# Performance work log

Hardware: AMD Instinct MI355X
Metric: run time of the kernel (lower is better)

Reference implementation:

```python
import jax, jax.numpy as jnp
import numpy as np

N = 100000
E = 3200000
G = 2000
EPS = 1e-5

def gcn_conv(x, W, b, src, dst):
    # PyG GCNConv: add self-loops, symmetric deg^-1/2 normalization,
    # out_i = sum_j norm_ij * (x_j @ W) + b
    loop = jnp.arange(N, dtype=src.dtype)
    s = jnp.concatenate([src, loop])
    d = jnp.concatenate([dst, loop])
    deg = jax.ops.segment_sum(jnp.ones_like(d, dtype=x.dtype), d, num_segments=N)
    dinv = jax.lax.rsqrt(jnp.maximum(deg, 1.0))
    norm = dinv[s] * dinv[d]                      # [E+N]
    h = x @ W                                     # [N, out]
    msg = h[s] * norm[:, None]                    # gather + scale
    return jax.ops.segment_sum(msg, d, num_segments=N) + b

def batchnorm(h, g, be):
    mu = jnp.mean(h, axis=0)
    var = jnp.mean((h - mu) ** 2, axis=0)
    return (h - mu) * jax.lax.rsqrt(var + EPS) * g + be

def setup_inputs() -> dict:
    key = jax.random.key(0)
    ks = jax.random.split(key, 16)
    inp = {
        "x": jax.random.normal(ks[0], (N, 10), dtype=jnp.float32),
        "src": jax.random.randint(ks[1], (E,), 0, N, dtype=jnp.int32),
        "dst": jax.random.randint(ks[2], (E,), 0, N, dtype=jnp.int32),
        "batch": jnp.sort(jax.random.randint(ks[3], (N,), 0, G, dtype=jnp.int32)),
        "W1": jax.random.normal(ks[4], (10, 64), dtype=jnp.float32) * 0.3,
        "b1": jnp.zeros((64,), jnp.float32),
        "g1": jnp.ones((64,), jnp.float32),
        "be1": jnp.zeros((64,), jnp.float32),
        "W2": jax.random.normal(ks[5], (64, 128), dtype=jnp.float32) * 0.12,
        "b2": jnp.zeros((128,), jnp.float32),
        "g2": jnp.ones((128,), jnp.float32),
        "be2": jnp.zeros((128,), jnp.float32),
        "fW1": jax.random.normal(ks[6], (128, 64), dtype=jnp.float32) * 0.09,
        "fb1": jnp.zeros((64,), jnp.float32),
        "fW2": jax.random.normal(ks[7], (64, 1), dtype=jnp.float32) * 0.12,
        "fb2": jnp.zeros((1,), jnp.float32),
    }
    return inp

def reference(x, src, dst, batch, W1, b1, g1, be1, W2, b2, g2, be2, fW1, fb1, fW2, fb2):
    h = jax.nn.relu(batchnorm(gcn_conv(x, W1, b1, src, dst), g1, be1))
    h = jax.nn.relu(batchnorm(gcn_conv(h, W2, b2, src, dst), g2, be2))
    # global_mean_pool over graphs
    s = jax.ops.segment_sum(h, batch, num_segments=G)
    cnt = jax.ops.segment_sum(jnp.ones((N,), h.dtype), batch, num_segments=G)
    pooled = s / jnp.maximum(cnt, 1.0)[:, None]   # [G, 128]
    # dropout is identity in eval mode
    h = jax.nn.relu(pooled @ fW1 + fb1)
    return h @ fW2 + fb2                          # [G, 1]
```

## Files before the change

kernel.cpp:

```cpp
#include <hip/hip_runtime.h>
#include <hip/hip_fp16.h>

#define NN 100000
#define NE 3200000
#define NG 2000
#define NB 391
#define BKT_SH 8
#define EPB 2048
#define EPT (EPB / 256)
#define PAD 16
#define CAP 10240
static constexpr float BN_EPS = 1e-5f;

typedef _Float16 f16x8 __attribute__((ext_vector_type(8)));
typedef float    f32x4 __attribute__((ext_vector_type(4)));

__global__ __launch_bounds__(1024) void k_init(int* bcur, float* s1, float* s2) {
    int t = threadIdx.x;
    if (t < NB) bcur[t * PAD] = t * CAP;
    if (t < 128) s1[t] = 0.f;
    if (t < 256) s2[t] = 0.f;
}

__global__ __launch_bounds__(256) void k_bucket(const int* __restrict__ src, const int* __restrict__ dst,
                                                int* __restrict__ bcur, int* __restrict__ stage) {
    __shared__ int cnt[NB];
    __shared__ int base[NB];
    int t = threadIdx.x;
    long long e0 = (long long)blockIdx.x * EPB;
    int ew[EPT], eb[EPT], lp[EPT];
#pragma unroll
    for (int i = 0; i < EPT; ++i) {
        long long e = e0 + t + i * 256;
        if (e < NE) {
            int d = dst[e];
            ew[i] = ((d & 255) << 17) | src[e];
            eb[i] = d >> BKT_SH;
        } else eb[i] = -1;
    }
    for (int i = t; i < NB; i += 256) cnt[i] = 0;
    __syncthreads();
#pragma unroll
    for (int i = 0; i < EPT; ++i)
        if (eb[i] >= 0) lp[i] = atomicAdd(&cnt[eb[i]], 1);
    __syncthreads();
    for (int i = t; i < NB; i += 256) {
        int c = cnt[i];
        base[i] = c ? atomicAdd(&bcur[i * PAD], c) : 0;
    }
    __syncthreads();
#pragma unroll
    for (int i = 0; i < EPT; ++i)
        if (eb[i] >= 0) stage[base[eb[i]] + lp[i]] = ew[i];
}

__global__ __launch_bounds__(256) void k_csr(const int* __restrict__ stage,
                                             const int* __restrict__ bcur, const float* __restrict__ x,
                                             int* __restrict__ deg_i, int* __restrict__ row_start,
                                             float* __restrict__ dinv, int* __restrict__ srcs,
                                             __half2* __restrict__ xh2) {
    __shared__ int ldeg[256];
    __shared__ int scn[256];
    __shared__ int lcur[256];
    int t = threadIdx.x;
    int b = blockIdx.x;
    int base = b * CAP;
    int end  = bcur[b * PAD];
    ldeg[t] = 0;
    __syncthreads();
    for (int e = base + t; e < end; e += 256)
        atomicAdd(&ldeg[(stage[e] >> 17) & 255], 1);
    __syncthreads();
    int v = ldeg[t];
    scn[t] = v;
    __syncthreads();
#pragma unroll
    for (int off = 1; off < 256; off <<= 1) {
        int a = (t >= off) ? scn[t - off] : 0;
        __syncthreads();
        scn[t] += a;
        __syncthreads();
    }
    int rs = base + scn[t] - v;
    lcur[t] = rs;
    int i = (b << BKT_SH) + t;
    if (i < NN) {
        deg_i[i] = v;
        row_start[i] = rs;
        float dv = rsqrtf((float)(v + 1));
        dinv[i] = dv;
        float xv[10];
#pragma unroll
        for (int k = 0; k < 10; ++k) xv[k] = x[i * 10 + k] * dv;
#pragma unroll
        for (int c = 0; c < 8; ++c) {
            float a = (2 * c < 10) ? xv[2 * c] : 0.f;
            float bb = (2 * c + 1 < 10) ? xv[2 * c + 1] : 0.f;
            xh2[i * 8 + c] = __floats2half2_rn(a, bb);
        }
    }
    __syncthreads();
    for (int e = base + t; e < end; e += 256) {
        int w = stage[e];
        int pos = atomicAdd(&lcur[(w >> 17) & 255], 1);
        srcs[pos] = w & 0x1FFFF;
    }
}

__global__ __launch_bounds__(256) void k_gather1(const __half2* __restrict__ xh2, const int* __restrict__ srcs,
                                                 const int* __restrict__ row_start, const int* __restrict__ deg,
                                                 const float* __restrict__ dinv, float2* __restrict__ aggx2) {
    int lane = threadIdx.x & 63;
    int wid  = threadIdx.x >> 6;
    int sub  = lane >> 3;
    int li   = lane & 7;
    int d = blockIdx.x * 32 + wid * 8 + sub;
    if (d >= NN) return;
    int start = row_start[d];
    int cnt   = deg[d];
    float ax = 0.f, ay = 0.f;
    int k = 0;
    for (; k + 4 <= cnt; k += 4) {
        int s0 = srcs[start + k];
        int s1 = srcs[start + k + 1];
        int s2 = srcs[start + k + 2];
        int s3 = srcs[start + k + 3];
        float2 u0 = __half22float2(xh2[s0 * 8 + li]);
        float2 u1 = __half22float2(xh2[s1 * 8 + li]);
        float2 u2 = __half22float2(xh2[s2 * 8 + li]);
        float2 u3 = __half22float2(xh2[s3 * 8 + li]);
        ax += (u0.x + u1.x) + (u2.x + u3.x);
        ay += (u0.y + u1.y) + (u2.y + u3.y);
    }
    for (; k < cnt; ++k) {
        int s = srcs[start + k];
        float2 u = __half22float2(xh2[s * 8 + li]);
        ax += u.x; ay += u.y;
    }
    {
        float2 u = __half22float2(xh2[d * 8 + li]);
        ax += u.x; ay += u.y;
    }
    float dd = dinv[d];
    aggx2[d * 8 + li] = make_float2(dd * ax, dd * ay);
}

__global__ __launch_bounds__(256) void k_mm1s(const float* __restrict__ aggx, const float* __restrict__ W,
                                              const float* __restrict__ b, __half* __restrict__ h1h,
                                              float* __restrict__ sums1) {
    __shared__ float ls[256];
    __shared__ float lq[256];
    int t = threadIdx.x;
    int rg = t >> 6;
    int f = t & 63;
    float w[10];
#pragma unroll
    for (int k = 0; k < 10; ++k) w[k] = W[k * 64 + f];
    float bf = b[f];
    float s = 0.f, q = 0.f;
    for (int row = blockIdx.x * 4 + rg; row < NN; row += 512 * 4) {
        float acc = bf;
#pragma unroll
        for (int k = 0; k < 10; ++k) acc += aggx[row * 16 + k] * w[k];
        s += acc; q += acc * acc;
        h1h[row * 64 + f] = __float2half(acc);
    }
    ls[t] = s; lq[t] = q;
    __syncthreads();
    if (t < 64) {
        float S = ls[t] + ls[t + 64] + ls[t + 128] + ls[t + 192];
        float Q = lq[t] + lq[t + 64] + lq[t + 128] + lq[t + 192];
        atomicAdd(&sums1[f], S);
        atomicAdd(&sums1[64 + f], Q);
    }
}

__global__ __launch_bounds__(256) void k_bn_apply1h(const float4* __restrict__ h1h4, const float* __restrict__ sums1,
                                                    const float* __restrict__ g, const float* __restrict__ be,
                                                    const float* __restrict__ dinv, int2* __restrict__ h1f8) {
    int idx = blockIdx.x * 256 + threadIdx.x;
    if (idx >= NN * 8) return;
    int i = idx >> 3;
    int c = idx & 7;
    const float invn = 1.0f / (float)NN;
    float dv = dinv[i];
    float4 r = h1h4[idx];
    const __half2* p = (const __half2*)&r;
    float rv[8];
#pragma unroll
    for (int j = 0; j < 4; ++j) {
        int f0 = 8 * c + 2 * j, f1 = f0 + 1;
        float mu0 = sums1[f0] * invn, mu1 = sums1[f1] * invn;
        float sc0 = g[f0] * rsqrtf(sums1[64 + f0] * invn - mu0 * mu0 + BN_EPS);
        float sc1 = g[f1] * rsqrtf(sums1[64 + f1] * invn - mu1 * mu1 + BN_EPS);
        float2 u = __half22float2(p[j]);
        rv[2 * j]     = fmaxf((u.x - mu0) * sc0 + be[f0], 0.f) * dv;
        rv[2 * j + 1] = fmaxf((u.y - mu1) * sc1 + be[f1], 0.f) * dv;
    }
    int lo = __builtin_amdgcn_cvt_pk_fp8_f32(rv[0], rv[1], 0, false);
    lo     = __builtin_amdgcn_cvt_pk_fp8_f32(rv[2], rv[3], lo, true);
    int hi = __builtin_amdgcn_cvt_pk_fp8_f32(rv[4], rv[5], 0, false);
    hi     = __builtin_amdgcn_cvt_pk_fp8_f32(rv[6], rv[7], hi, true);
    h1f8[idx] = make_int2(lo, hi);
}

__global__ __launch_bounds__(256) void k_gather2(const int* __restrict__ h1f8i, const int* __restrict__ srcs,
                                                 const int* __restrict__ row_start, const int* __restrict__ deg,
                                                 const float* __restrict__ dinv, float2* __restrict__ aggh2) {
    int lane = threadIdx.x & 63;
    int wid  = threadIdx.x >> 6;
    int sub  = lane >> 4;
    int li   = lane & 15;
    int d = blockIdx.x * 16 + wid * 4 + sub;
    if (d >= NN) return;
    int start = row_start[d];
    int cnt   = deg[d];
    float a0 = 0.f, a1 = 0.f, a2 = 0.f, a3 = 0.f;
    int k = 0;
    for (; k + 8 <= cnt; k += 8) {
        int s[8], w[8];
#pragma unroll
        for (int j = 0; j < 8; ++j) s[j] = srcs[start + k + j];
#pragma unroll
        for (int j = 0; j < 8; ++j) w[j] = h1f8i[s[j] * 16 + li];
#pragma unroll
        for (int j = 0; j < 8; ++j) {
            auto lo = __builtin_amdgcn_cvt_pk_f32_fp8(w[j], false);
            auto hi = __builtin_amdgcn_cvt_pk_f32_fp8(w[j], true);
            a0 += lo[0]; a1 += lo[1]; a2 += hi[0]; a3 += hi[1];
        }
    }
    for (; k < cnt; ++k) {
        int w = h1f8i[srcs[start + k] * 16 + li];
        auto lo = __builtin_amdgcn_cvt_pk_f32_fp8(w, false);
        auto hi = __builtin_amdgcn_cvt_pk_f32_fp8(w, true);
        a0 += lo[0]; a1 += lo[1]; a2 += hi[0]; a3 += hi[1];
    }
    {
        int w = h1f8i[d * 16 + li];
        auto lo = __builtin_amdgcn_cvt_pk_f32_fp8(w, false);
        auto hi = __builtin_amdgcn_cvt_pk_f32_fp8(w, true);
        a0 += lo[0]; a1 += lo[1]; a2 += hi[0]; a3 += hi[1];
    }
    float dd = dinv[d];
    __half2 o[2];
    o[0] = __floats2half2_rn(dd * a0, dd * a1);
    o[1] = __floats2half2_rn(dd * a2, dd * a3);
    aggh2[d * 16 + li] = *(const float2*)o;
}

__global__ __launch_bounds__(256) void k_mm2m(const __half* __restrict__ aggh, const float* __restrict__ W,
                                              const float* __restrict__ b, __half* __restrict__ h2,
                                              float* __restrict__ sums2) {
    int t = threadIdx.x;
    __shared__ _Float16 w2h[64 * 128];
    for (int i = t; i < 64 * 128; i += 256) w2h[i] = (_Float16)W[i];
    __syncthreads();

    int lane = t & 63;
    int wid  = t >> 6;
    int quad = lane >> 4;
    int n16  = lane & 15;

    f16x8 bfr[8][2];
#pragma unroll
    for (int nt = 0; nt < 8; ++nt)
#pragma unroll
        for (int kk = 0; kk < 2; ++kk)
#pragma unroll
            for (int j = 0; j < 8; ++j)
                bfr[nt][kk][j] = w2h[(kk * 32 + quad * 8 + j) * 128 + nt * 16 + n16];
    float bcol[8];
#pragma unroll
    for (int nt = 0; nt < 8; ++nt) bcol[nt] = b[nt * 16 + n16];

    const f16x8* a8 = (const f16x8*)aggh;
    float s[8] = {0.f}, q[8] = {0.f};

    for (int rt = blockIdx.x * 4 + wid; rt < NN / 16; rt += 256 * 4) {
        int arow = rt * 16 + n16;
        f16x8 a0 = a8[arow * 8 + quad];
        f16x8 a1 = a8[arow * 8 + 4 + quad];
#pragma unroll
        for (int nt = 0; nt < 8; ++nt) {
            f32x4 c = {0.f, 0.f, 0.f, 0.f};
            c = __builtin_amdgcn_mfma_f32_16x16x32_f16(a0, bfr[nt][0], c, 0, 0, 0);
            c = __builtin_amdgcn_mfma_f32_16x16x32_f16(a1, bfr[nt][1], c, 0, 0, 0);
            float bb = bcol[nt];
#pragma unroll
            for (int reg = 0; reg < 4; ++reg) {
                float v = c[reg] + bb;
                s[nt] += v; q[nt] += v * v;
                int row = rt * 16 + quad * 4 + reg;
                h2[(long long)row * 128 + nt * 16 + n16] = __float2half(v);
            }
        }
    }
#pragma unroll
    for (int nt = 0; nt < 8; ++nt) {
        s[nt] += __shfl_xor(s[nt], 16, 64); s[nt] += __shfl_xor(s[nt], 32, 64);
        q[nt] += __shfl_xor(q[nt], 16, 64); q[nt] += __shfl_xor(q[nt], 32, 64);
    }
    __shared__ float lsS[4][128];
    __shared__ float lsQ[4][128];
    if (lane < 16) {
#pragma unroll
        for (int nt = 0; nt < 8; ++nt) {
            lsS[wid][nt * 16 + lane] = s[nt];
            lsQ[wid][nt * 16 + lane] = q[nt];
        }
    }
    __syncthreads();
    if (t < 128) {
        float S = lsS[0][t] + lsS[1][t] + lsS[2][t] + lsS[3][t];
        float Q = lsQ[0][t] + lsQ[1][t] + lsQ[2][t] + lsQ[3][t];
        atomicAdd(&sums2[t], S);
        atomicAdd(&sums2[128 + t], Q);
    }
}

__global__ __launch_bounds__(128) void k_pool(const __half* __restrict__ h2, const float* __restrict__ sums2,
                                              const float* __restrict__ g, const float* __restrict__ be,
                                              const int* __restrict__ batch, float* __restrict__ pooled) {
    int gb = blockIdx.x;
    int f = threadIdx.x;
    int lo = 0, hi = NN;
    while (lo < hi) { int mid = (lo + hi) >> 1; if (batch[mid] < gb) lo = mid + 1; else hi = mid; }
    int start = lo;
    hi = NN;
    while (lo < hi) { int mid = (lo + hi) >> 1; if (batch[mid] < gb + 1) lo = mid + 1; else hi = mid; }
    int end = lo;

    const float invn = 1.0f / (float)NN;
    float mu = sums2[f] * invn;
    float sc = g[f] * rsqrtf(sums2[128 + f] * invn - mu * mu + BN_EPS);
    float bb = be[f];
    float acc = 0.f;
    for (int i = start; i < end; ++i) {
        float v = __half2float(h2[(long long)i * 128 + f]);
        acc += fmaxf((v - mu) * sc + bb, 0.f);
    }
    float inv = 1.0f / fmaxf((float)(end - start), 1.0f);
    pooled[gb * 128 + f] = acc * inv;
}

__global__ __launch_bounds__(64) void k_mlp(const float* __restrict__ pooled,
                                            const float* __restrict__ fW1, const float* __restrict__ fb1,
                                            const float* __restrict__ fW2, const float* __restrict__ fb2,
                                            float* __restrict__ out) {
    int g = blockIdx.x;
    int j = threadIdx.x;
    float acc = fb1[j];
#pragma unroll
    for (int k = 0; k < 128; ++k) acc += pooled[g * 128 + k] * fW1[k * 64 + j];
    float hj = fmaxf(acc, 0.f) * fW2[j];
#pragma unroll
    for (int off = 32; off > 0; off >>= 1) hj += __shfl_down(hj, off, 64);
    if (j == 0) out[g] = hj + fb2[0];
}

extern "C" void kernel_launch(void* const* d_in, const int* in_sizes, int n_in,
                              void* d_out, int out_size, void* d_ws, size_t ws_size,
                              hipStream_t stream) {
    const float* x    = (const float*)d_in[0];
    const int*   src  = (const int*)d_in[1];
    const int*   dst  = (const int*)d_in[2];
    const int*   batch= (const int*)d_in[3];
    const float* W1   = (const float*)d_in[4];
    const float* b1   = (const float*)d_in[5];
    const float* g1   = (const float*)d_in[6];
    const float* be1  = (const float*)d_in[7];
    const float* W2   = (const float*)d_in[8];
    const float* b2   = (const float*)d_in[9];
    const float* g2   = (const float*)d_in[10];
    const float* be2  = (const float*)d_in[11];
    const float* fW1  = (const float*)d_in[12];
    const float* fb1  = (const float*)d_in[13];
    const float* fW2  = (const float*)d_in[14];
    const float* fb2  = (const float*)d_in[15];
    float* out = (float*)d_out;

    float* ws        = (float*)d_ws;
    int*   deg_i     = (int*)ws;
    int*   row_start = deg_i + NN;
    float* dinv      = (float*)(row_start + NN);
    int*   bcur      = (int*)(dinv + NN);
    float* sums1     = (float*)(bcur + NB * PAD);
    float* sums2     = sums1 + 128;
    float* h1R       = sums2 + 256;
    float* agghR     = h1R + NN * 64;
    float* h2R       = agghR + NN * 64;
    __half2* xh2     = (__half2*)h1R;
    __half*  h1h     = (__half*)h1R;
    float*   pooled  = h1R;
    int*     stage   = (int*)agghR;
    __half*  aggh    = (__half*)agghR;
    float*   aggx    = h2R;
    int*     srcs    = (int*)(h2R + NN * 16);
    int2*    h1f8    = (int2*)(h2R + NN * 16 + NB * CAP);
    __half*  h2      = (__half*)h2R;

    k_init<<<1, 1024, 0, stream>>>(bcur, sums1, sums2);
    k_bucket<<<(NE + EPB - 1) / EPB, 256, 0, stream>>>(src, dst, bcur, stage);
    k_csr<<<NB, 256, 0, stream>>>(stage, bcur, x, deg_i, row_start, dinv, srcs, xh2);

    k_gather1<<<(NN + 31) / 32, 256, 0, stream>>>(xh2, srcs, row_start, deg_i, dinv, (float2*)aggx);
    k_mm1s<<<512, 256, 0, stream>>>(aggx, W1, b1, h1h, sums1);
    k_bn_apply1h<<<(NN * 8 + 255) / 256, 256, 0, stream>>>((const float4*)h1h, sums1, g1, be1, dinv, h1f8);

    k_gather2<<<(NN + 15) / 16, 256, 0, stream>>>((const int*)h1f8, srcs, row_start, deg_i, dinv, (float2*)aggh);
    k_mm2m<<<256, 256, 0, stream>>>(aggh, W2, b2, h2, sums2);

    k_pool<<<NG, 128, 0, stream>>>(h2, sums2, g2, be2, batch, pooled);
    k_mlp<<<NG, 64, 0, stream>>>(pooled, fW1, fb1, fW2, fb2, out);
}
```

Before: 344.2 us.

## Sort edges by bucket in shared memory before scattering to staging

The bucketing kernel now handles twice as many edges per block and performs a local counting sort in LDS. It does an exclusive prefix scan over the per-bucket counts, places edges contiguously by bucket in shared memory, then writes them out in order, so consecutive threads store to consecutive addresses within each bucket's region. This is meant to make the scattered global stores to the staging array coalesced and to halve the number of global atomics per edge. The cost is extra LDS traffic, an additional scan and barriers, and fewer blocks in flight.

```diff
diff --git a/kernel.cpp b/kernel.cpp
--- a/kernel.cpp
+++ b/kernel.cpp
@@ -6,7 +6,7 @@
 #define NG 2000
 #define NB 391
 #define BKT_SH 8
-#define EPB 2048
+#define EPB 4096
 #define EPT (EPB / 256)
 #define PAD 16
 #define CAP 10240
@@ -26,32 +26,71 @@
                                                 int* __restrict__ bcur, int* __restrict__ stage) {
     __shared__ int cnt[NB];
     __shared__ int base[NB];
+    __shared__ int eidx[EPB];
+    __shared__ unsigned short ebkt[EPB];
     int t = threadIdx.x;
     long long e0 = (long long)blockIdx.x * EPB;
-    int ew[EPT], eb[EPT], lp[EPT];
+    int ew[EPT]; short eb[EPT]; short lp[EPT];
 #pragma unroll
     for (int i = 0; i < EPT; ++i) {
         long long e = e0 + t + i * 256;
         if (e < NE) {
             int d = dst[e];
             ew[i] = ((d & 255) << 17) | src[e];
-            eb[i] = d >> BKT_SH;
+            eb[i] = (short)(d >> BKT_SH);
         } else eb[i] = -1;
     }
     for (int i = t; i < NB; i += 256) cnt[i] = 0;
     __syncthreads();
 #pragma unroll
     for (int i = 0; i < EPT; ++i)
-        if (eb[i] >= 0) lp[i] = atomicAdd(&cnt[eb[i]], 1);
+        if (eb[i] >= 0) lp[i] = (short)atomicAdd(&cnt[eb[i]], 1);
     __syncthreads();
     for (int i = t; i < NB; i += 256) {
         int c = cnt[i];
         base[i] = c ? atomicAdd(&bcur[i * PAD], c) : 0;
     }
     __syncthreads();
-#pragma unroll
-    for (int i = 0; i < EPT; ++i)
-        if (eb[i] >= 0) stage[base[eb[i]] + lp[i]] = ew[i];
+    if (t < 64) {
+        int idx0 = t * 7;
+        int vals[7];
+        int s = 0;
+#pragma unroll
+        for (int j = 0; j < 7; ++j) {
+            int ii = idx0 + j;
+            vals[j] = (ii < NB) ? cnt[ii] : 0;
+            s += vals[j];
+        }
+        int incl = s;
+#pragma unroll
+        for (int off = 1; off < 64; off <<= 1) {
+            int v = __shfl_up(incl, off, 64);
+            if (t >= off) incl += v;
+        }
+        int run = incl - s;
+#pragma unroll
+        for (int j = 0; j < 7; ++j) {
+            int ii = idx0 + j;
+            if (ii < NB) { cnt[ii] = run; run += vals[j]; }
+        }
+    }
+    __syncthreads();
+#pragma unroll
+    for (int i = 0; i < EPT; ++i) {
+        if (eb[i] >= 0) {
+            int p = cnt[eb[i]] + lp[i];
+            eidx[p] = ew[i];
+            ebkt[p] = (unsigned short)eb[i];
+        }
+    }
+    __syncthreads();
+    long long eend = min((long long)NE, e0 + EPB);
+    int total = (int)(eend - e0);
+    for (int j = t; j < total; j += 256) {
+        int w = eidx[j];
+        int b = ebkt[j];
+        stage[base[b] + (j - cnt[b])] = w;
+    }
 }
 
 __global__ __launch_bounds__(256) void k_csr(const int* __restrict__ stage,
```

New measurement: 319.7 us. 7.1% less time.
